# Kernel tuning notes

Measured on AMD Instinct MI355X. Metric: run time of the kernel, lower is better.

## Reference

```python
import jax, jax.numpy as jnp
import numpy as np

N = 62        # EEG channels (nodes)
B = 4096      # batch of graphs
F_IN = 5      # DE features per node
HID = 400     # SGConv output dim
OUT = 2       # classes


def setup_inputs() -> dict:
    key = jax.random.key(0)
    ks = jax.random.split(key, 5)
    xs, ys = np.tril_indices(N)                      # learnable lower-tri edge weights
    src = np.repeat(np.arange(N), N)                 # dense graph, row-major edge order
    dst = np.tile(np.arange(N), N)
    return {
        "X": jax.random.normal(ks[0], (B, N, F_IN), jnp.float32),
        "X2": jnp.zeros((B, 1), jnp.float32),                      # unused by forward
        "edge_w_tril": jax.random.normal(ks[1], (xs.size,), jnp.float32) * 0.1 + 0.5,
        "lin_w": jax.random.normal(ks[2], (F_IN, HID), jnp.float32) / np.sqrt(F_IN),
        "lin_b": jnp.zeros((HID,), jnp.float32),
        "fc_w": jax.random.normal(ks[3], (HID, OUT), jnp.float32) / np.sqrt(HID),
        "fc_b": jnp.zeros((OUT,), jnp.float32),
        "src": jnp.asarray(src, dtype=jnp.int32),
        "dst": jnp.asarray(dst, dtype=jnp.int32),
        "tril_x": jnp.asarray(xs, dtype=jnp.int32),
        "tril_y": jnp.asarray(ys, dtype=jnp.int32),
        "padding_masks": jnp.ones((B, N), dtype=bool),             # unused by forward
    }


def reference(X, X2, edge_w_tril, lin_w, lin_b, fc_w, fc_b,
              src, dst, tril_x, tril_y, padding_masks):
    # Rebuild symmetric dense weight matrix from lower-tri parameters
    W = jnp.zeros((N, N), X.dtype).at[tril_x, tril_y].set(edge_w_tril)
    W = W + W.T - jnp.diag(jnp.diag(W))
    ew = W.reshape(-1)  # edge order matches (src outer, dst inner); self-loops already present

    # SGConv norm: deg scatter over source rows with |w|, D^-1/2 W D^-1/2
    deg = jnp.zeros((N,), X.dtype).at[src].add(jnp.abs(ew))
    deg_safe = jnp.where(deg > 0, deg, 1.0)
    dinv = jnp.where(deg > 0, deg_safe ** -0.5, 0.0)
    norm = dinv[src] * ew * dinv[dst]  # [E]

    # propagate: gather -> scale -> scatter-add at targets, K=2 hops (batched over B)
    def prop(x):  # x: [B, N, F]
        msg = norm[None, :, None] * x[:, src, :]       # [B, E, F]
        return jnp.zeros_like(x).at[:, dst, :].add(msg)

    x = prop(prop(X))
    h = jax.nn.relu(x @ lin_w + lin_b)   # relu(lin(.)) as in forward: [B, N, HID]
    pooled = h.sum(axis=1)               # global_add_pool over nodes: [B, HID]
    # dropout p=0.7 skipped (eval mode / deterministic reference)
    return pooled @ fc_w + fc_b          # [B, 2]
```

## Files before the change

### kernel.cpp

```cpp
#include <hip/hip_runtime.h>
#include <hip/hip_bf16.h>

#define NNODE 62
#define FIN 5
#define HID 400
#define NTRIL 1953
#define MST 63
#define WST 72
#define WAVES 8

typedef __attribute__((ext_vector_type(8))) short bf16x8;
typedef __attribute__((ext_vector_type(4))) float f32x4;

static __device__ __forceinline__ short f2bf(float x) {
    __hip_bfloat16 h = __float2bfloat16(x);
    return *reinterpret_cast<short*>(&h);
}

__global__ __launch_bounds__(512, 4) void rgnn_fused(
        const float* __restrict__ X,     const float* __restrict__ ew,
        const int* __restrict__ tx,      const int* __restrict__ ty,
        const float* __restrict__ lin_w, const float* __restrict__ lin_b,
        const float* __restrict__ fc_w,  const float* __restrict__ fc_b,
        float* __restrict__ out, int B) {
    __shared__ float Wn[NNODE * MST];
    __shared__ float dinv[64];
    __shared__ __align__(16) short Wfrag[8][64][8];
    __shared__ __align__(16) short lwT[HID][8];
    __shared__ float fcs[HID * 2];
    __shared__ __align__(16) short XT[WAVES][FIN][WST];
    __shared__ __align__(16) short Y2A[WAVES][64][8];
    __shared__ __align__(16) short Zs[8];

    const int t = threadIdx.x;
    const int w = t >> 6;
    const int lane = t & 63;
    const int b = blockIdx.x * WAVES + w;

    for (int i = t; i < NNODE * MST; i += 512) Wn[i] = 0.f;
    if (t < 64) dinv[t] = 0.f;
    for (int i = t; i < HID * 8; i += 512) {
        const int c = i >> 3, k = i & 7;
        float v = 0.f;
        if (k < FIN) v = lin_w[k * HID + c];
        else if (k == FIN) v = lin_b[c];
        lwT[c][k] = f2bf(v);
    }
    for (int i = t; i < HID * 2; i += 512) fcs[i] = fc_w[i];
    if (t < 8) Zs[t] = 0;
    for (int i = t; i < WAVES * 64 * 8; i += 512) {
        const int n = (i >> 3) & 63, k = i & 7;
        ((short*)Y2A)[i] = (k == FIN && n < NNODE) ? (short)0x3F80 : (short)0;
    }
    for (int i = t; i < WAVES * FIN * WST; i += 512) ((short*)XT)[i] = 0;
    __syncthreads();

    for (int e = t; e < NTRIL; e += 512) {
        const int x = tx[e], y = ty[e];
        const float v = ew[e];
        Wn[x * MST + y] = v;
        Wn[y * MST + x] = v;
    }
    if (b < B) {
        const float* xb = X + (size_t)b * (NNODE * FIN);
        for (int idx = lane; idx < NNODE * FIN; idx += 64) {
            const int n = idx / FIN, f = idx - n * FIN;
            XT[w][f][n] = f2bf(xb[idx]);
        }
    }
    __syncthreads();

    if (t < NNODE * 8) {
        const int r = t >> 3, j = t & 7;
        float s = 0.f;
        for (int k = j; k < NNODE; k += 8) s += fabsf(Wn[r * MST + k]);
        s += __shfl_xor(s, 4);
        s += __shfl_xor(s, 2);
        s += __shfl_xor(s, 1);
        if (j == 0) dinv[r] = (s > 0.f) ? (1.0f / sqrtf(s)) : 0.f;
    }
    __syncthreads();

    for (int i = t; i < NNODE * MST; i += 512) {
        const int r = i / MST, c = i - r * MST;
        Wn[i] = Wn[i] * dinv[r] * dinv[c];
    }
    __syncthreads();

    {
        const int fi = t >> 6, l = t & 63;
        const int rt = fi >> 1, ks = fi & 1;
        const int row = (l & 15) + 16 * rt;
        const int k0 = ks * 32 + (l >> 4) * 8;
        union { short s[8]; bf16x8 v8; } u;
        #pragma unroll
        for (int j = 0; j < 8; ++j) {
            const int k = k0 + j;
            u.s[j] = (row < NNODE && k < NNODE) ? f2bf(Wn[row * MST + k]) : (short)0;
        }
        *(bf16x8*)&Wfrag[fi][l][0] = u.v8;
    }
    __syncthreads();

    if (b >= B) return;

    bf16x8 wf[8];
    #pragma unroll
    for (int fi = 0; fi < 8; ++fi) wf[fi] = *(const bf16x8*)&Wfrag[fi][lane][0];

    const int f16 = lane & 15;
    const int g   = lane >> 4;
    const bool freal = (f16 < FIN);
    const short* zp = &Zs[0];
    const f32x4 z4 = {0.f, 0.f, 0.f, 0.f};

    bf16x8 bx0, bx1;
    {
        const short* p0 = freal ? &XT[w][f16][g * 8]      : zp;
        const short* p1 = freal ? &XT[w][f16][32 + g * 8] : zp;
        bx0 = *(const bf16x8*)p0;
        bx1 = *(const bf16x8*)p1;
    }
    f32x4 acc[4];
    #pragma unroll
    for (int rt = 0; rt < 4; ++rt) {
        acc[rt] = __builtin_amdgcn_mfma_f32_16x16x32_bf16(wf[rt * 2 + 0], bx0, z4, 0, 0, 0);
        acc[rt] = __builtin_amdgcn_mfma_f32_16x16x32_bf16(wf[rt * 2 + 1], bx1, acc[rt], 0, 0, 0);
    }
    if (freal) {
        #pragma unroll
        for (int rt = 0; rt < 4; ++rt) {
            const int n0 = rt * 16 + g * 4;
            const unsigned int d0 = (unsigned short)f2bf(acc[rt][0]) |
                                    ((unsigned int)(unsigned short)f2bf(acc[rt][1]) << 16);
            const unsigned int d1 = (unsigned short)f2bf(acc[rt][2]) |
                                    ((unsigned int)(unsigned short)f2bf(acc[rt][3]) << 16);
            if (n0 + 1 < NNODE) *(unsigned int*)&XT[w][f16][n0] = d0;
            if (n0 + 3 < NNODE) *(unsigned int*)&XT[w][f16][n0 + 2] = d1;
        }
    }

    {
        const short* p0 = freal ? &XT[w][f16][g * 8]      : zp;
        const short* p1 = freal ? &XT[w][f16][32 + g * 8] : zp;
        bx0 = *(const bf16x8*)p0;
        bx1 = *(const bf16x8*)p1;
    }
    #pragma unroll
    for (int rt = 0; rt < 4; ++rt) {
        acc[rt] = __builtin_amdgcn_mfma_f32_16x16x32_bf16(wf[rt * 2 + 0], bx0, z4, 0, 0, 0);
        acc[rt] = __builtin_amdgcn_mfma_f32_16x16x32_bf16(wf[rt * 2 + 1], bx1, acc[rt], 0, 0, 0);
    }
    if (freal) {
        #pragma unroll
        for (int rt = 0; rt < 4; ++rt) {
            const int n0 = rt * 16 + g * 4;
            #pragma unroll
            for (int r = 0; r < 4; ++r) {
                if (n0 + r < NNODE) Y2A[w][n0 + r][f16] = f2bf(acc[rt][r]);
            }
        }
    }

    bf16x8 af[4];
    #pragma unroll
    for (int rt = 0; rt < 4; ++rt) {
        const short* ap = (lane < 16) ? &Y2A[w][lane + 16 * rt][0] : zp;
        af[rt] = *(const bf16x8*)ap;
    }

    float o0 = 0.f, o1 = 0.f;
    for (int ct = 0; ct < 25; ++ct) {
        const short* bp = (lane < 16) ? &lwT[16 * ct + f16][0] : zp;
        const bf16x8 bfr = *(const bf16x8*)bp;
        const float2 fw = *(const float2*)&fcs[(16 * ct + f16) * 2];
        const f32x4 ac0 = __builtin_amdgcn_mfma_f32_16x16x32_bf16(af[0], bfr, z4, 0, 0, 0);
        const f32x4 ac1 = __builtin_amdgcn_mfma_f32_16x16x32_bf16(af[1], bfr, z4, 0, 0, 0);
        const f32x4 ac2 = __builtin_amdgcn_mfma_f32_16x16x32_bf16(af[2], bfr, z4, 0, 0, 0);
        const f32x4 ac3 = __builtin_amdgcn_mfma_f32_16x16x32_bf16(af[3], bfr, z4, 0, 0, 0);
        float p0 = fmaxf(ac0[0], 0.f) + fmaxf(ac0[1], 0.f) + fmaxf(ac0[2], 0.f) + fmaxf(ac0[3], 0.f);
        float p1 = fmaxf(ac1[0], 0.f) + fmaxf(ac1[1], 0.f) + fmaxf(ac1[2], 0.f) + fmaxf(ac1[3], 0.f);
        float p2 = fmaxf(ac2[0], 0.f) + fmaxf(ac2[1], 0.f) + fmaxf(ac2[2], 0.f) + fmaxf(ac2[3], 0.f);
        float p3 = fmaxf(ac3[0], 0.f) + fmaxf(ac3[1], 0.f) + fmaxf(ac3[2], 0.f) + fmaxf(ac3[3], 0.f);
        const float pc = (p0 + p1) + (p2 + p3);
        o0 = fmaf(pc, fw.x, o0);
        o1 = fmaf(pc, fw.y, o1);
    }
    #pragma unroll
    for (int s = 32; s > 0; s >>= 1) {
        o0 += __shfl_xor(o0, s, 64);
        o1 += __shfl_xor(o1, s, 64);
    }
    if (lane == 0) {
        out[2 * b + 0] = o0 + fc_b[0];
        out[2 * b + 1] = o1 + fc_b[1];
    }
}

extern "C" void kernel_launch(void* const* d_in, const int* in_sizes, int n_in,
                              void* d_out, int out_size, void* d_ws, size_t ws_size,
                              hipStream_t stream) {
    const float* X     = (const float*)d_in[0];
    const float* ew    = (const float*)d_in[2];
    const float* lin_w = (const float*)d_in[3];
    const float* lin_b = (const float*)d_in[4];
    const float* fc_w  = (const float*)d_in[5];
    const float* fc_b  = (const float*)d_in[6];
    const int*   tx    = (const int*)d_in[9];
    const int*   ty    = (const int*)d_in[10];

    float* outp = (float*)d_out;
    const int B = in_sizes[0] / (NNODE * FIN);

    rgnn_fused<<<(B + WAVES - 1) / WAVES, 512, 0, stream>>>(
        X, ew, tx, ty, lin_w, lin_b, fc_w, fc_b, outp, B);
}
```

Baseline: 23.59 us.

## Process two graphs per wave and fold normalization into fragment build

```diff
diff --git a/kernel.cpp b/kernel.cpp
--- a/kernel.cpp
+++ b/kernel.cpp
@@ -8,6 +8,7 @@
 #define MST 63
 #define WST 72
 #define WAVES 8
+#define GPW 2
 
 typedef __attribute__((ext_vector_type(8))) short bf16x8;
 typedef __attribute__((ext_vector_type(4))) float f32x4;
@@ -17,28 +18,26 @@
     return *reinterpret_cast<short*>(&h);
 }
 
-__global__ __launch_bounds__(512, 4) void rgnn_fused(
+__global__ __launch_bounds__(512, 2) void rgnn_fused(
         const float* __restrict__ X,     const float* __restrict__ ew,
         const int* __restrict__ tx,      const int* __restrict__ ty,
         const float* __restrict__ lin_w, const float* __restrict__ lin_b,
         const float* __restrict__ fc_w,  const float* __restrict__ fc_b,
         float* __restrict__ out, int B) {
     __shared__ float Wn[NNODE * MST];
-    __shared__ float dinv[64];
+    __shared__ float dinv[NNODE];
     __shared__ __align__(16) short Wfrag[8][64][8];
     __shared__ __align__(16) short lwT[HID][8];
     __shared__ float fcs[HID * 2];
-    __shared__ __align__(16) short XT[WAVES][FIN][WST];
-    __shared__ __align__(16) short Y2A[WAVES][64][8];
+    __shared__ __align__(16) short XT[WAVES][GPW][FIN][WST];
+    __shared__ __align__(16) short Y2A[WAVES][GPW][64][8];
     __shared__ __align__(16) short Zs[8];
 
     const int t = threadIdx.x;
     const int w = t >> 6;
     const int lane = t & 63;
-    const int b = blockIdx.x * WAVES + w;
-
-    for (int i = t; i < NNODE * MST; i += 512) Wn[i] = 0.f;
-    if (t < 64) dinv[t] = 0.f;
+    const int bbase = blockIdx.x * (WAVES * GPW) + w * GPW;
+
     for (int i = t; i < HID * 8; i += 512) {
         const int c = i >> 3, k = i & 7;
         float v = 0.f;
@@ -48,25 +47,26 @@
     }
     for (int i = t; i < HID * 2; i += 512) fcs[i] = fc_w[i];
     if (t < 8) Zs[t] = 0;
-    for (int i = t; i < WAVES * 64 * 8; i += 512) {
-        const int n = (i >> 3) & 63, k = i & 7;
-        ((short*)Y2A)[i] = (k == FIN && n < NNODE) ? (short)0x3F80 : (short)0;
-    }
-    for (int i = t; i < WAVES * FIN * WST; i += 512) ((short*)XT)[i] = 0;
-    __syncthreads();
-
     for (int e = t; e < NTRIL; e += 512) {
         const int x = tx[e], y = ty[e];
         const float v = ew[e];
         Wn[x * MST + y] = v;
         Wn[y * MST + x] = v;
     }
-    if (b < B) {
-        const float* xb = X + (size_t)b * (NNODE * FIN);
-        for (int idx = lane; idx < NNODE * FIN; idx += 64) {
-            const int n = idx / FIN, f = idx - n * FIN;
-            XT[w][f][n] = f2bf(xb[idx]);
-        }
+    #pragma unroll
+    for (int gg = 0; gg < GPW; ++gg) {
+        const int b = bbase + gg;
+        if (b < B) {
+            const float* xb = X + (size_t)b * (NNODE * FIN);
+            for (int idx = lane; idx < NNODE * FIN; idx += 64) {
+                const int n = idx / FIN, f = idx - n * FIN;
+                XT[w][gg][f][n] = f2bf(xb[idx]);
+            }
+        }
+    }
+    if (lane < GPW * FIN) {
+        const int gg = lane / FIN, f = lane - gg * FIN;
+        *(unsigned int*)&XT[w][gg][f][62] = 0u;
     }
     __syncthreads();
 
@@ -78,12 +78,6 @@
         s += __shfl_xor(s, 2);
         s += __shfl_xor(s, 1);
         if (j == 0) dinv[r] = (s > 0.f) ? (1.0f / sqrtf(s)) : 0.f;
-    }
-    __syncthreads();
-
-    for (int i = t; i < NNODE * MST; i += 512) {
-        const int r = i / MST, c = i - r * MST;
-        Wn[i] = Wn[i] * dinv[r] * dinv[c];
     }
     __syncthreads();
 
@@ -96,13 +90,14 @@
         #pragma unroll
         for (int j = 0; j < 8; ++j) {
             const int k = k0 + j;
-            u.s[j] = (row < NNODE && k < NNODE) ? f2bf(Wn[row * MST + k]) : (short)0;
+            u.s[j] = (row < NNODE && k < NNODE)
+                   ? f2bf(Wn[row * MST + k] * dinv[row] * dinv[k]) : (short)0;
         }
         *(bf16x8*)&Wfrag[fi][l][0] = u.v8;
     }
     __syncthreads();
 
-    if (b >= B) return;
+    if (bbase >= B) return;
 
     bf16x8 wf[8];
     #pragma unroll
@@ -110,14 +105,16 @@
 
     const int f16 = lane & 15;
     const int g   = lane >> 4;
-    const bool freal = (f16 < FIN);
+    const int dsel = f16 >> 3;
+    const int dk   = f16 & 7;
+    const bool fr  = (dk < FIN);
     const short* zp = &Zs[0];
     const f32x4 z4 = {0.f, 0.f, 0.f, 0.f};
 
     bf16x8 bx0, bx1;
     {
-        const short* p0 = freal ? &XT[w][f16][g * 8]      : zp;
-        const short* p1 = freal ? &XT[w][f16][32 + g * 8] : zp;
+        const short* p0 = fr ? &XT[w][dsel][dk][g * 8]      : zp;
+        const short* p1 = fr ? &XT[w][dsel][dk][32 + g * 8] : zp;
         bx0 = *(const bf16x8*)p0;
         bx1 = *(const bf16x8*)p1;
     }
@@ -127,7 +124,7 @@
         acc[rt] = __builtin_amdgcn_mfma_f32_16x16x32_bf16(wf[rt * 2 + 0], bx0, z4, 0, 0, 0);
         acc[rt] = __builtin_amdgcn_mfma_f32_16x16x32_bf16(wf[rt * 2 + 1], bx1, acc[rt], 0, 0, 0);
     }
-    if (freal) {
+    if (fr) {
         #pragma unroll
         for (int rt = 0; rt < 4; ++rt) {
             const int n0 = rt * 16 + g * 4;
@@ -135,14 +132,14 @@
                                     ((unsigned int)(unsigned short)f2bf(acc[rt][1]) << 16);
             const unsigned int d1 = (unsigned short)f2bf(acc[rt][2]) |
                                     ((unsigned int)(unsigned short)f2bf(acc[rt][3]) << 16);
-            if (n0 + 1 < NNODE) *(unsigned int*)&XT[w][f16][n0] = d0;
-            if (n0 + 3 < NNODE) *(unsigned int*)&XT[w][f16][n0 + 2] = d1;
+            if (n0 + 1 < NNODE) *(unsigned int*)&XT[w][dsel][dk][n0] = d0;
+            if (n0 + 3 < NNODE) *(unsigned int*)&XT[w][dsel][dk][n0 + 2] = d1;
         }
     }
 
     {
-        const short* p0 = freal ? &XT[w][f16][g * 8]      : zp;
-        const short* p1 = freal ? &XT[w][f16][32 + g * 8] : zp;
+        const short* p0 = fr ? &XT[w][dsel][dk][g * 8]      : zp;
+        const short* p1 = fr ? &XT[w][dsel][dk][32 + g * 8] : zp;
         bx0 = *(const bf16x8*)p0;
         bx1 = *(const bf16x8*)p1;
     }
@@ -151,49 +148,72 @@
         acc[rt] = __builtin_amdgcn_mfma_f32_16x16x32_bf16(wf[rt * 2 + 0], bx0, z4, 0, 0, 0);
         acc[rt] = __builtin_amdgcn_mfma_f32_16x16x32_bf16(wf[rt * 2 + 1], bx1, acc[rt], 0, 0, 0);
     }
-    if (freal) {
+    #pragma unroll
+    for (int rt = 0; rt < 4; ++rt) {
+        const int n0 = rt * 16 + g * 4;
         #pragma unroll
-        for (int rt = 0; rt < 4; ++rt) {
-            const int n0 = rt * 16 + g * 4;
-            #pragma unroll
-            for (int r = 0; r < 4; ++r) {
-                if (n0 + r < NNODE) Y2A[w][n0 + r][f16] = f2bf(acc[rt][r]);
+        for (int r = 0; r < 4; ++r) {
+            const int n = n0 + r;
+            short val = 0;
+            if (n < NNODE) {
+                val = (dk < FIN) ? f2bf(acc[rt][r])
+                                 : ((dk == FIN) ? (short)0x3F80 : (short)0);
             }
-        }
-    }
-
-    bf16x8 af[4];
-    #pragma unroll
-    for (int rt = 0; rt < 4; ++rt) {
-        const short* ap = (lane < 16) ? &Y2A[w][lane + 16 * rt][0] : zp;
-        af[rt] = *(const bf16x8*)ap;
-    }
-
-    float o0 = 0.f, o1 = 0.f;
+            Y2A[w][dsel][n][dk] = val;
+        }
+    }
+
+    bf16x8 af0[4], af1[4];
+    #pragma unroll
+    for (int rt = 0; rt < 4; ++rt) {
+        const short* a0 = (lane < 16) ? &Y2A[w][0][lane + 16 * rt][0] : zp;
+        const short* a1 = (lane < 16) ? &Y2A[w][1][lane + 16 * rt][0] : zp;
+        af0[rt] = *(const bf16x8*)a0;
+        af1[rt] = *(const bf16x8*)a1;
+    }
+
+    float o0a = 0.f, o1a = 0.f, o0b = 0.f, o1b = 0.f;
     for (int ct = 0; ct < 25; ++ct) {
         const short* bp = (lane < 16) ? &lwT[16 * ct + f16][0] : zp;
         const bf16x8 bfr = *(const bf16x8*)bp;
         const float2 fw = *(const float2*)&fcs[(16 * ct + f16) * 2];
-        const f32x4 ac0 = __builtin_amdgcn_mfma_f32_16x16x32_bf16(af[0], bfr, z4, 0, 0, 0);
-        const f32x4 ac1 = __builtin_amdgcn_mfma_f32_16x16x32_bf16(af[1], bfr, z4, 0, 0, 0);
-        const f32x4 ac2 = __builtin_amdgcn_mfma_f32_16x16x32_bf16(af[2], bfr, z4, 0, 0, 0);
-        const f32x4 ac3 = __builtin_amdgcn_mfma_f32_16x16x32_bf16(af[3], bfr, z4, 0, 0, 0);
-        float p0 = fmaxf(ac0[0], 0.f) + fmaxf(ac0[1], 0.f) + fmaxf(ac0[2], 0.f) + fmaxf(ac0[3], 0.f);
-        float p1 = fmaxf(ac1[0], 0.f) + fmaxf(ac1[1], 0.f) + fmaxf(ac1[2], 0.f) + fmaxf(ac1[3], 0.f);
-        float p2 = fmaxf(ac2[0], 0.f) + fmaxf(ac2[1], 0.f) + fmaxf(ac2[2], 0.f) + fmaxf(ac2[3], 0.f);
-        float p3 = fmaxf(ac3[0], 0.f) + fmaxf(ac3[1], 0.f) + fmaxf(ac3[2], 0.f) + fmaxf(ac3[3], 0.f);
-        const float pc = (p0 + p1) + (p2 + p3);
-        o0 = fmaf(pc, fw.x, o0);
-        o1 = fmaf(pc, fw.y, o1);
+        const f32x4 a0 = __builtin_amdgcn_mfma_f32_16x16x32_bf16(af0[0], bfr, z4, 0, 0, 0);
+        const f32x4 b0 = __builtin_amdgcn_mfma_f32_16x16x32_bf16(af1[0], bfr, z4, 0, 0, 0);
+        const f32x4 a1 = __builtin_amdgcn_mfma_f32_16x16x32_bf16(af0[1], bfr, z4, 0, 0, 0);
+        const f32x4 b1 = __builtin_amdgcn_mfma_f32_16x16x32_bf16(af1[1], bfr, z4, 0, 0, 0);
+        const f32x4 a2 = __builtin_amdgcn_mfma_f32_16x16x32_bf16(af0[2], bfr, z4, 0, 0, 0);
+        const f32x4 b2 = __builtin_amdgcn_mfma_f32_16x16x32_bf16(af1[2], bfr, z4, 0, 0, 0);
+        const f32x4 a3 = __builtin_amdgcn_mfma_f32_16x16x32_bf16(af0[3], bfr, z4, 0, 0, 0);
+        const f32x4 b3 = __builtin_amdgcn_mfma_f32_16x16x32_bf16(af1[3], bfr, z4, 0, 0, 0);
+        float pa0 = fmaxf(a0[0],0.f)+fmaxf(a0[1],0.f)+fmaxf(a0[2],0.f)+fmaxf(a0[3],0.f);
+        float pa1 = fmaxf(a1[0],0.f)+fmaxf(a1[1],0.f)+fmaxf(a1[2],0.f)+fmaxf(a1[3],0.f);
+        float pa2 = fmaxf(a2[0],0.f)+fmaxf(a2[1],0.f)+fmaxf(a2[2],0.f)+fmaxf(a2[3],0.f);
+        float pa3 = fmaxf(a3[0],0.f)+fmaxf(a3[1],0.f)+fmaxf(a3[2],0.f)+fmaxf(a3[3],0.f);
+        float pb0 = fmaxf(b0[0],0.f)+fmaxf(b0[1],0.f)+fmaxf(b0[2],0.f)+fmaxf(b0[3],0.f);
+        float pb1 = fmaxf(b1[0],0.f)+fmaxf(b1[1],0.f)+fmaxf(b1[2],0.f)+fmaxf(b1[3],0.f);
+        float pb2 = fmaxf(b2[0],0.f)+fmaxf(b2[1],0.f)+fmaxf(b2[2],0.f)+fmaxf(b2[3],0.f);
+        float pb3 = fmaxf(b3[0],0.f)+fmaxf(b3[1],0.f)+fmaxf(b3[2],0.f)+fmaxf(b3[3],0.f);
+        const float pca = (pa0 + pa1) + (pa2 + pa3);
+        const float pcb = (pb0 + pb1) + (pb2 + pb3);
+        o0a = fmaf(pca, fw.x, o0a);
+        o1a = fmaf(pca, fw.y, o1a);
+        o0b = fmaf(pcb, fw.x, o0b);
+        o1b = fmaf(pcb, fw.y, o1b);
     }
     #pragma unroll
     for (int s = 32; s > 0; s >>= 1) {
-        o0 += __shfl_xor(o0, s, 64);
-        o1 += __shfl_xor(o1, s, 64);
+        o0a += __shfl_xor(o0a, s, 64);
+        o1a += __shfl_xor(o1a, s, 64);
+        o0b += __shfl_xor(o0b, s, 64);
+        o1b += __shfl_xor(o1b, s, 64);
     }
     if (lane == 0) {
-        out[2 * b + 0] = o0 + fc_b[0];
-        out[2 * b + 1] = o1 + fc_b[1];
+        out[2 * bbase + 0] = o0a + fc_b[0];
+        out[2 * bbase + 1] = o1a + fc_b[1];
+        if (bbase + 1 < B) {
+            out[2 * bbase + 2] = o0b + fc_b[0];
+            out[2 * bbase + 3] = o1b + fc_b[1];
+        }
     }
 }
 
@@ -212,6 +232,7 @@
     float* outp = (float*)d_out;
     const int B = in_sizes[0] / (NNODE * FIN);
 
-    rgnn_fused<<<(B + WAVES - 1) / WAVES, 512, 0, stream>>>(
+    const int gpb = WAVES * GPW;
+    rgnn_fused<<<(B + gpb - 1) / gpb, 512, 0, stream>>>(
         X, ew, tx, ty, lin_w, lin_b, fc_w, fc_b, outp, B);
 }
```

Measured after the change: 22.11 us. -6.3%, faster.

## Double graphs per block and drop redundant zero-init and barrier phases

Applied to the files above, without the earlier changes.

```diff
diff --git a/kernel.cpp b/kernel.cpp
--- a/kernel.cpp
+++ b/kernel.cpp
@@ -7,7 +7,7 @@
 #define NTRIL 1953
 #define MST 63
 #define WST 72
-#define WAVES 8
+#define WAVES 16
 
 typedef __attribute__((ext_vector_type(8))) short bf16x8;
 typedef __attribute__((ext_vector_type(4))) float f32x4;
@@ -17,7 +17,7 @@
     return *reinterpret_cast<short*>(&h);
 }
 
-__global__ __launch_bounds__(512, 4) void rgnn_fused(
+__global__ __launch_bounds__(1024, 4) void rgnn_fused(
         const float* __restrict__ X,     const float* __restrict__ ew,
         const int* __restrict__ tx,      const int* __restrict__ ty,
         const float* __restrict__ lin_w, const float* __restrict__ lin_b,
@@ -37,25 +37,16 @@
     const int lane = t & 63;
     const int b = blockIdx.x * WAVES + w;
 
-    for (int i = t; i < NNODE * MST; i += 512) Wn[i] = 0.f;
-    if (t < 64) dinv[t] = 0.f;
-    for (int i = t; i < HID * 8; i += 512) {
+    for (int i = t; i < HID * 8; i += 1024) {
         const int c = i >> 3, k = i & 7;
         float v = 0.f;
         if (k < FIN) v = lin_w[k * HID + c];
         else if (k == FIN) v = lin_b[c];
         lwT[c][k] = f2bf(v);
     }
-    for (int i = t; i < HID * 2; i += 512) fcs[i] = fc_w[i];
+    for (int i = t; i < HID * 2; i += 1024) fcs[i] = fc_w[i];
     if (t < 8) Zs[t] = 0;
-    for (int i = t; i < WAVES * 64 * 8; i += 512) {
-        const int n = (i >> 3) & 63, k = i & 7;
-        ((short*)Y2A)[i] = (k == FIN && n < NNODE) ? (short)0x3F80 : (short)0;
-    }
-    for (int i = t; i < WAVES * FIN * WST; i += 512) ((short*)XT)[i] = 0;
-    __syncthreads();
-
-    for (int e = t; e < NTRIL; e += 512) {
+    for (int e = t; e < NTRIL; e += 1024) {
         const int x = tx[e], y = ty[e];
         const float v = ew[e];
         Wn[x * MST + y] = v;
@@ -67,13 +58,15 @@
             const int n = idx / FIN, f = idx - n * FIN;
             XT[w][f][n] = f2bf(xb[idx]);
         }
+        if (lane < FIN) *(unsigned int*)&XT[w][lane][62] = 0u;
     }
     __syncthreads();
 
-    if (t < NNODE * 8) {
-        const int r = t >> 3, j = t & 7;
+    if (t < NNODE * 16) {
+        const int r = t >> 4, j = t & 15;
         float s = 0.f;
-        for (int k = j; k < NNODE; k += 8) s += fabsf(Wn[r * MST + k]);
+        for (int k = j; k < NNODE; k += 16) s += fabsf(Wn[r * MST + k]);
+        s += __shfl_xor(s, 8);
         s += __shfl_xor(s, 4);
         s += __shfl_xor(s, 2);
         s += __shfl_xor(s, 1);
@@ -81,13 +74,7 @@
     }
     __syncthreads();
 
-    for (int i = t; i < NNODE * MST; i += 512) {
-        const int r = i / MST, c = i - r * MST;
-        Wn[i] = Wn[i] * dinv[r] * dinv[c];
-    }
-    __syncthreads();
-
-    {
+    if (t < 512) {
         const int fi = t >> 6, l = t & 63;
         const int rt = fi >> 1, ks = fi & 1;
         const int row = (l & 15) + 16 * rt;
@@ -96,7 +83,8 @@
         #pragma unroll
         for (int j = 0; j < 8; ++j) {
             const int k = k0 + j;
-            u.s[j] = (row < NNODE && k < NNODE) ? f2bf(Wn[row * MST + k]) : (short)0;
+            u.s[j] = (row < NNODE && k < NNODE)
+                   ? f2bf(Wn[row * MST + k] * dinv[row] * dinv[k]) : (short)0;
         }
         *(bf16x8*)&Wfrag[fi][l][0] = u.v8;
     }
@@ -110,14 +98,14 @@
 
     const int f16 = lane & 15;
     const int g   = lane >> 4;
-    const bool freal = (f16 < FIN);
+    const bool fr = (f16 < FIN);
     const short* zp = &Zs[0];
     const f32x4 z4 = {0.f, 0.f, 0.f, 0.f};
 
     bf16x8 bx0, bx1;
     {
-        const short* p0 = freal ? &XT[w][f16][g * 8]      : zp;
-        const short* p1 = freal ? &XT[w][f16][32 + g * 8] : zp;
+        const short* p0 = fr ? &XT[w][f16][g * 8]      : zp;
+        const short* p1 = fr ? &XT[w][f16][32 + g * 8] : zp;
         bx0 = *(const bf16x8*)p0;
         bx1 = *(const bf16x8*)p1;
     }
@@ -127,7 +115,7 @@
         acc[rt] = __builtin_amdgcn_mfma_f32_16x16x32_bf16(wf[rt * 2 + 0], bx0, z4, 0, 0, 0);
         acc[rt] = __builtin_amdgcn_mfma_f32_16x16x32_bf16(wf[rt * 2 + 1], bx1, acc[rt], 0, 0, 0);
     }
-    if (freal) {
+    if (fr) {
         #pragma unroll
         for (int rt = 0; rt < 4; ++rt) {
             const int n0 = rt * 16 + g * 4;
@@ -141,8 +129,8 @@
     }
 
     {
-        const short* p0 = freal ? &XT[w][f16][g * 8]      : zp;
-        const short* p1 = freal ? &XT[w][f16][32 + g * 8] : zp;
+        const short* p0 = fr ? &XT[w][f16][g * 8]      : zp;
+        const short* p1 = fr ? &XT[w][f16][32 + g * 8] : zp;
         bx0 = *(const bf16x8*)p0;
         bx1 = *(const bf16x8*)p1;
     }
@@ -151,13 +139,19 @@
         acc[rt] = __builtin_amdgcn_mfma_f32_16x16x32_bf16(wf[rt * 2 + 0], bx0, z4, 0, 0, 0);
         acc[rt] = __builtin_amdgcn_mfma_f32_16x16x32_bf16(wf[rt * 2 + 1], bx1, acc[rt], 0, 0, 0);
     }
-    if (freal) {
+    if (f16 < 8) {
         #pragma unroll
         for (int rt = 0; rt < 4; ++rt) {
             const int n0 = rt * 16 + g * 4;
             #pragma unroll
             for (int r = 0; r < 4; ++r) {
-                if (n0 + r < NNODE) Y2A[w][n0 + r][f16] = f2bf(acc[rt][r]);
+                const int n = n0 + r;
+                short val = 0;
+                if (n < NNODE) {
+                    val = (f16 < FIN) ? f2bf(acc[rt][r])
+                                      : ((f16 == FIN) ? (short)0x3F80 : (short)0);
+                }
+                Y2A[w][n][f16] = val;
             }
         }
     }
@@ -178,10 +172,10 @@
         const f32x4 ac1 = __builtin_amdgcn_mfma_f32_16x16x32_bf16(af[1], bfr, z4, 0, 0, 0);
         const f32x4 ac2 = __builtin_amdgcn_mfma_f32_16x16x32_bf16(af[2], bfr, z4, 0, 0, 0);
         const f32x4 ac3 = __builtin_amdgcn_mfma_f32_16x16x32_bf16(af[3], bfr, z4, 0, 0, 0);
-        float p0 = fmaxf(ac0[0], 0.f) + fmaxf(ac0[1], 0.f) + fmaxf(ac0[2], 0.f) + fmaxf(ac0[3], 0.f);
-        float p1 = fmaxf(ac1[0], 0.f) + fmaxf(ac1[1], 0.f) + fmaxf(ac1[2], 0.f) + fmaxf(ac1[3], 0.f);
-        float p2 = fmaxf(ac2[0], 0.f) + fmaxf(ac2[1], 0.f) + fmaxf(ac2[2], 0.f) + fmaxf(ac2[3], 0.f);
-        float p3 = fmaxf(ac3[0], 0.f) + fmaxf(ac3[1], 0.f) + fmaxf(ac3[2], 0.f) + fmaxf(ac3[3], 0.f);
+        float p0 = fmaxf(ac0[0],0.f)+fmaxf(ac0[1],0.f)+fmaxf(ac0[2],0.f)+fmaxf(ac0[3],0.f);
+        float p1 = fmaxf(ac1[0],0.f)+fmaxf(ac1[1],0.f)+fmaxf(ac1[2],0.f)+fmaxf(ac1[3],0.f);
+        float p2 = fmaxf(ac2[0],0.f)+fmaxf(ac2[1],0.f)+fmaxf(ac2[2],0.f)+fmaxf(ac2[3],0.f);
+        float p3 = fmaxf(ac3[0],0.f)+fmaxf(ac3[1],0.f)+fmaxf(ac3[2],0.f)+fmaxf(ac3[3],0.f);
         const float pc = (p0 + p1) + (p2 + p3);
         o0 = fmaf(pc, fw.x, o0);
         o1 = fmaf(pc, fw.y, o1);
@@ -212,6 +206,6 @@
     float* outp = (float*)d_out;
     const int B = in_sizes[0] / (NNODE * FIN);
 
-    rgnn_fused<<<(B + WAVES - 1) / WAVES, 512, 0, stream>>>(
+    rgnn_fused<<<(B + WAVES - 1) / WAVES, 1024, 0, stream>>>(
         X, ew, tx, ty, lin_w, lin_b, fc_w, fc_b, outp, B);
 }
```

Measured after the change: 20.88 us. -11.5%, faster.
